# Performance work log

Measured on AMD Instinct MI355X. Metric: run time of the kernel, lower is better.

## Reference

```python
import jax, jax.numpy as jnp
import numpy as np

B, T, C = 8, 1024, 1024
EPS = 1e-5
NEG_INF = -1e38


def layernorm(x, w, b):
    mu = jnp.mean(x, axis=-1, keepdims=True)
    var = jnp.var(x, axis=-1, keepdims=True)
    return (x - mu) * jax.lax.rsqrt(var + EPS) * w + b


def wkv_scan(w, u, k, v):
    """Numerically-stable RWKV-4 WKV recurrence (forward direction).
    w: [C] (negative decay), u: [C] bonus, k, v: [B, T, C]. Returns [B, T, C]."""
    kt = jnp.swapaxes(k, 0, 1)  # [T, B, C]
    vt = jnp.swapaxes(v, 0, 1)
    bsz = k.shape[0]
    a0 = jnp.zeros((bsz, C), k.dtype)
    b0 = jnp.zeros((bsz, C), k.dtype)
    p0 = jnp.full((bsz, C), NEG_INF, k.dtype)

    def step(carry, inp):
        a, b, p = carry
        kk, vv = inp
        # output at current step (with bonus u on current token)
        q = jnp.maximum(p, u + kk)
        e1 = jnp.exp(p - q)
        e2 = jnp.exp(u + kk - q)
        out = (e1 * a + e2 * vv) / (e1 * b + e2)
        # decay state and absorb current token
        q2 = jnp.maximum(p + w, kk)
        f1 = jnp.exp(p + w - q2)
        f2 = jnp.exp(kk - q2)
        return (f1 * a + f2 * vv, f1 * b + f2, q2), out

    _, outs = jax.lax.scan(step, (a0, b0, p0), (kt, vt))
    return jnp.swapaxes(outs, 0, 1)  # [B, T, C]


def setup_inputs() -> dict:
    key = jax.random.key(0)
    ks = jax.random.split(key, 12)
    s = 0.02
    d = {}
    d["x"] = jax.random.normal(ks[0], (B, T, C), jnp.float32)
    d["ln1_w"] = jnp.ones((C,), jnp.float32)
    d["ln1_b"] = jnp.zeros((C,), jnp.float32)
    d["ln2_w"] = jnp.ones((C,), jnp.float32)
    d["ln2_b"] = jnp.zeros((C,), jnp.float32)
    d["Wr"] = jax.random.normal(ks[1], (C, C), jnp.float32) * s
    d["Wk"] = jax.random.normal(ks[2], (C, C), jnp.float32) * s
    d["Wv"] = jax.random.normal(ks[3], (C, C), jnp.float32) * s
    d["Wo"] = jax.random.normal(ks[4], (C, C), jnp.float32) * s
    d["decay"] = jax.random.normal(ks[5], (C,), jnp.float32) * 0.1
    d["u"] = jax.random.normal(ks[6], (C,), jnp.float32) * 0.1
    d["Wfk"] = jax.random.normal(ks[7], (4 * C, C), jnp.float32) * s
    d["Wfv"] = jax.random.normal(ks[8], (C, 4 * C), jnp.float32) * s
    d["Wfr"] = jax.random.normal(ks[9], (C, C), jnp.float32) * s
    return d


def reference(x, ln1_w, ln1_b, ln2_w, ln2_b, Wr, Wk, Wv, Wo, decay, u, Wfk, Wfv, Wfr):
    # --- bidirectional time-mix (WKV attention) ---
    xn = layernorm(x, ln1_w, ln1_b)
    r = jax.nn.sigmoid(xn @ Wr.T)
    k = xn @ Wk.T
    v = xn @ Wv.T
    w = -jnp.exp(decay)  # per-channel negative decay
    wkv_f = wkv_scan(w, u, k, v)
    wkv_b = jnp.flip(wkv_scan(w, u, jnp.flip(k, axis=1), jnp.flip(v, axis=1)), axis=1)
    wkv = 0.5 * (wkv_f + wkv_b)
    x = x + (r * wkv) @ Wo.T
    # --- channel-mix FFN ---
    xn2 = layernorm(x, ln2_w, ln2_b)
    kk = jnp.square(jax.nn.relu(xn2 @ Wfk.T))  # [B, T, 4C]
    x = x + jax.nn.sigmoid(xn2 @ Wfr.T) * (kk @ Wfv.T)
    return x
```

## Files before the change

### kernel.cpp

```cpp
#include <hip/hip_runtime.h>
#include <cstdint>
#include <cstddef>

typedef unsigned short u16;
typedef unsigned char u8;
typedef unsigned int u32;
typedef __bf16 bf16_t;
typedef bf16_t bf16x8 __attribute__((ext_vector_type(8)));
typedef float f32x4 __attribute__((ext_vector_type(4)));
typedef int i32x8 __attribute__((ext_vector_type(8)));

#define GCH 16
#define TCH 64

static __device__ __forceinline__ float bf2f(u16 v) {
    union { unsigned int u; float f; } cv;
    cv.u = ((unsigned int)v) << 16;
    return cv.f;
}
static __device__ __forceinline__ u16 f2bf(float f) {
    union { float f; unsigned int u; } cv;
    cv.f = f;
    unsigned int r = 0x7fffu + ((cv.u >> 16) & 1u);
    return (u16)((cv.u + r) >> 16);
}

#define SBAR() do { __builtin_amdgcn_sched_barrier(0); \
                    __builtin_amdgcn_s_barrier();      \
                    __builtin_amdgcn_sched_barrier(0); } while (0)

struct WSegs { const float* src[7]; void* dst[7]; int n4[7]; int mode[7]; };

__global__ __launch_bounds__(256)
void wconv_all(WSegs s)
{
    const int seg = blockIdx.y;
    const int i = blockIdx.x * 256 + threadIdx.x;
    if (i >= s.n4[seg]) return;
    float4 f = ((const float4*)s.src[seg])[i];
    if (s.mode[seg] == 0) {
        ushort4 o;
        o.x = f2bf(f.x); o.y = f2bf(f.y); o.z = f2bf(f.z); o.w = f2bf(f.w);
        ((ushort4*)s.dst[seg])[i] = o;
    } else {
        const int p0 = __builtin_amdgcn_cvt_pk_fp8_f32(f.x * 16.f, f.y * 16.f, 0, 0);
        const int p1 = __builtin_amdgcn_cvt_pk_fp8_f32(f.z * 16.f, f.w * 16.f, 0, 0);
        ((u32*)s.dst[seg])[i] = (u32)(p0 & 0xFFFF) | ((u32)p1 << 16);
    }
}

template<int BF16IN, int OUT8>
__global__ __launch_bounds__(256)
void ln_kernel(const void* __restrict__ xin, const float* __restrict__ w,
               const float* __restrict__ b, void* __restrict__ out)
{
    const int row = blockIdx.x;
    const int tid = threadIdx.x;
    float vals[4];
    if (BF16IN) {
        const ushort4 uv = ((const ushort4*)((const u16*)xin + (size_t)row * 1024))[tid];
        vals[0] = bf2f(uv.x); vals[1] = bf2f(uv.y);
        vals[2] = bf2f(uv.z); vals[3] = bf2f(uv.w);
    } else {
        const float4 f = ((const float4*)((const float*)xin + (size_t)row * 1024))[tid];
        vals[0] = f.x; vals[1] = f.y; vals[2] = f.z; vals[3] = f.w;
    }
    float s  = vals[0] + vals[1] + vals[2] + vals[3];
    float ss = vals[0]*vals[0] + vals[1]*vals[1] + vals[2]*vals[2] + vals[3]*vals[3];
    for (int off = 32; off; off >>= 1) {
        s  += __shfl_down(s, off, 64);
        ss += __shfl_down(ss, off, 64);
    }
    __shared__ float redS[4], redQ[4];
    if ((tid & 63) == 0) { redS[tid >> 6] = s; redQ[tid >> 6] = ss; }
    __syncthreads();
    s  = redS[0] + redS[1] + redS[2] + redS[3];
    ss = redQ[0] + redQ[1] + redQ[2] + redQ[3];
    const float mu  = s * (1.f / 1024.f);
    const float var = ss * (1.f / 1024.f) - mu * mu;
    const float rs  = rsqrtf(var + 1e-5f);
    const float4 wv = ((const float4*)w)[tid];
    const float4 bv = ((const float4*)b)[tid];
    const float o0 = (vals[0] - mu) * rs * wv.x + bv.x;
    const float o1 = (vals[1] - mu) * rs * wv.y + bv.y;
    const float o2 = (vals[2] - mu) * rs * wv.z + bv.z;
    const float o3 = (vals[3] - mu) * rs * wv.w + bv.w;
    if (OUT8) {
        const int p0 = __builtin_amdgcn_cvt_pk_fp8_f32(o0, o1, 0, 0);
        const int p1 = __builtin_amdgcn_cvt_pk_fp8_f32(o2, o3, 0, 0);
        ((u32*)out)[(size_t)row * 256 + tid] = (u32)(p0 & 0xFFFF) | ((u32)p1 << 16);
    } else {
        ushort4 o;
        o.x = f2bf(o0); o.y = f2bf(o1); o.z = f2bf(o2); o.w = f2bf(o3);
        ((ushort4*)out)[(size_t)row * 256 + tid] = o;
    }
}

template<int EPI, int DBUF>
__global__ __launch_bounds__(256)
void gemm_bt(const u16* __restrict__ A, const u16* __restrict__ B,
             int M, int N, int K,
             void* __restrict__ outp,
             const void* __restrict__ aux1, const void* __restrict__ aux2)
{
    __shared__ u16 lA[(1 + DBUF) * 128 * 64];
    __shared__ u16 lB[(1 + DBUF) * 128 * 64];
    const int tid  = threadIdx.x;
    const int wave = tid >> 6;
    const int lane = tid & 63;
    const int q    = lane >> 4;
    const int l16  = lane & 15;
    const long mBase = (long)blockIdx.x * 128;
    const long nBase = (long)blockIdx.y * 128;
    const int wm = (wave >> 1) * 64;
    const int wn = (wave & 1) * 64;

    f32x4 acc[4][4];
#pragma unroll
    for (int i = 0; i < 4; ++i)
#pragma unroll
        for (int j = 0; j < 4; ++j)
#pragma unroll
            for (int r = 0; r < 4; ++r) acc[i][j][r] = 0.f;

    const int srow = tid >> 3;
    const int scol = ((tid & 7) ^ (srow & 7)) * 8;
    const int ldsW = wave * 512;
    const int swz = l16 & 7;

    if (DBUF == 0) {
        for (int kb = 0; kb < K; kb += 64) {
            __syncthreads();
#pragma unroll
            for (int c = 0; c < 4; ++c) {
                const int row = c * 32 + srow;
                const u16* ga = A + (mBase + row) * (long)K + kb + scol;
                const u16* gb = B + (nBase + row) * (long)K + kb + scol;
                __builtin_amdgcn_global_load_lds(
                    (const __attribute__((address_space(1))) void*)ga,
                    (__attribute__((address_space(3))) void*)(lA + c * 2048 + ldsW),
                    16, 0, 0);
                __builtin_amdgcn_global_load_lds(
                    (const __attribute__((address_space(1))) void*)gb,
                    (__attribute__((address_space(3))) void*)(lB + c * 2048 + ldsW),
                    16, 0, 0);
            }
            __syncthreads();
#pragma unroll
            for (int ks = 0; ks < 2; ++ks) {
                const int grp = ((ks * 4 + q) ^ swz) * 8;
                bf16x8 af[4], bfm[4];
#pragma unroll
                for (int i = 0; i < 4; ++i) {
                    af[i]  = *(const bf16x8*)(lA + (wm + i * 16 + l16) * 64 + grp);
                    bfm[i] = *(const bf16x8*)(lB + (wn + i * 16 + l16) * 64 + grp);
                }
#pragma unroll
                for (int i = 0; i < 4; ++i)
#pragma unroll
                    for (int j = 0; j < 4; ++j)
                        acc[i][j] = __builtin_amdgcn_mfma_f32_16x16x32_bf16(
                            af[i], bfm[j], acc[i][j], 0, 0, 0);
            }
        }
    } else {
        auto stage = [&](int kb, int bufsel) {
#pragma unroll
            for (int c = 0; c < 4; ++c) {
                const int row = c * 32 + srow;
                const u16* ga = A + (mBase + row) * (long)K + kb + scol;
                const u16* gb = B + (nBase + row) * (long)K + kb + scol;
                __builtin_amdgcn_global_load_lds(
                    (const __attribute__((address_space(1))) void*)ga,
                    (__attribute__((address_space(3))) void*)(lA + bufsel * 8192 + c * 2048 + ldsW),
                    16, 0, 0);
                __builtin_amdgcn_global_load_lds(
                    (const __attribute__((address_space(1))) void*)gb,
                    (__attribute__((address_space(3))) void*)(lB + bufsel * 8192 + c * 2048 + ldsW),
                    16, 0, 0);
            }
        };
        auto compute = [&](int bufsel) {
            const u16* bA = lA + bufsel * 8192;
            const u16* bB = lB + bufsel * 8192;
#pragma unroll
            for (int ks = 0; ks < 2; ++ks) {
                const int grp = ((ks * 4 + q) ^ swz) * 8;
                bf16x8 af[4], bfm[4];
#pragma unroll
                for (int i = 0; i < 4; ++i) {
                    af[i]  = *(const bf16x8*)(bA + (wm + i * 16 + l16) * 64 + grp);
                    bfm[i] = *(const bf16x8*)(bB + (wn + i * 16 + l16) * 64 + grp);
                }
#pragma unroll
                for (int i = 0; i < 4; ++i)
#pragma unroll
                    for (int j = 0; j < 4; ++j)
                        acc[i][j] = __builtin_amdgcn_mfma_f32_16x16x32_bf16(
                            af[i], bfm[j], acc[i][j], 0, 0, 0);
            }
        };

        const int nt = K >> 6;
        stage(0, 0);
        stage(64, 1);
        asm volatile("s_waitcnt vmcnt(8)" ::: "memory");
        SBAR();
        for (int t = 0; t < nt - 2; ++t) {
            compute(t & 1);
            SBAR();
            stage((t + 2) << 6, t & 1);
            asm volatile("s_waitcnt vmcnt(8)" ::: "memory");
            SBAR();
        }
        compute(nt & 1);
        asm volatile("s_waitcnt vmcnt(0)" ::: "memory");
        SBAR();
        compute((nt - 1) & 1);
    }

    if (EPI == 5) {
        const long seg = nBase >> 10;
        u16* optr = (u16*)(seg == 0 ? outp : seg == 1 ? (void*)aux1 : (void*)aux2);
        const long cb = (nBase & 1023) + wn + l16;
#pragma unroll
        for (int i = 0; i < 4; ++i)
#pragma unroll
            for (int r = 0; r < 4; ++r) {
                const long rowOff = (mBase + wm + i * 16 + q * 4 + r) * 1024 + cb;
#pragma unroll
                for (int j = 0; j < 4; ++j)
                    optr[rowOff + j * 16] = f2bf(acc[i][j][r]);
            }
    } else {
        const long colBase = nBase + wn + l16;
#pragma unroll
        for (int i = 0; i < 4; ++i) {
#pragma unroll
            for (int r = 0; r < 4; ++r) {
                const long row = mBase + wm + i * 16 + q * 4 + r;
                const long rowOff = row * (long)N;
#pragma unroll
                for (int j = 0; j < 4; ++j) {
                    const long idx = rowOff + colBase + j * 16;
                    const float val = acc[i][j][r];
                    if (EPI == 1) {
                        ((u16*)outp)[idx] = f2bf(((const float*)aux1)[idx] + val);
                    } else {
                        const float t = bf2f(((const u16*)aux1)[idx])
                                      + bf2f(((const u16*)aux2)[idx]) * val;
                        ((float*)outp)[idx] = t;
                    }
                }
            }
        }
    }
}

__global__ __launch_bounds__(256)
void gemm_f8(const u8* __restrict__ A, const u8* __restrict__ B,
             int M, int N, int K,
             u16* __restrict__ kk, u16* __restrict__ rp)
{
    __shared__ __align__(16) u8 lA[128 * 128];
    __shared__ __align__(16) u8 lB[128 * 128];
    const int tid  = threadIdx.x;
    const int wave = tid >> 6;
    const int lane = tid & 63;
    const int q    = lane >> 4;
    const int l16  = lane & 15;
    const long mBase = (long)blockIdx.x * 128;
    const long nBase = (long)blockIdx.y * 128;
    const int wm = (wave >> 1) * 64;
    const int wn = (wave & 1) * 64;

    f32x4 acc[4][4];
#pragma unroll
    for (int i = 0; i < 4; ++i)
#pragma unroll
        for (int j = 0; j < 4; ++j)
#pragma unroll
            for (int r = 0; r < 4; ++r) acc[i][j][r] = 0.f;

    const int srow  = tid >> 3;
    const int scolB = ((tid & 7) ^ (srow & 7)) * 16;
    const int ldsW  = wave * 1024;
    const int swz   = l16 & 7;

    for (int kb = 0; kb < K; kb += 128) {
        __syncthreads();
#pragma unroll
        for (int c = 0; c < 4; ++c) {
            const int row = c * 32 + srow;
            const u8* ga = A + (mBase + row) * (long)K + kb + scolB;
            const u8* gb = B + (nBase + row) * (long)K + kb + scolB;
            __builtin_amdgcn_global_load_lds(
                (const __attribute__((address_space(1))) void*)ga,
                (__attribute__((address_space(3))) void*)(lA + c * 4096 + ldsW),
                16, 0, 0);
            __builtin_amdgcn_global_load_lds(
                (const __attribute__((address_space(1))) void*)gb,
                (__attribute__((address_space(3))) void*)(lB + c * 4096 + ldsW),
                16, 0, 0);
        }
        __syncthreads();
        const int u0 = ((2 * q) ^ swz) * 16;
        const int u1 = ((2 * q + 1) ^ swz) * 16;
        i32x8 af[4], bfm[4];
#pragma unroll
        for (int i = 0; i < 4; ++i) {
            {
                const u8* base = lA + (wm + i * 16 + l16) * 128;
                const uint4 lo = *(const uint4*)(base + u0);
                const uint4 hi = *(const uint4*)(base + u1);
                af[i][0] = lo.x; af[i][1] = lo.y; af[i][2] = lo.z; af[i][3] = lo.w;
                af[i][4] = hi.x; af[i][5] = hi.y; af[i][6] = hi.z; af[i][7] = hi.w;
            }
            {
                const u8* base = lB + (wn + i * 16 + l16) * 128;
                const uint4 lo = *(const uint4*)(base + u0);
                const uint4 hi = *(const uint4*)(base + u1);
                bfm[i][0] = lo.x; bfm[i][1] = lo.y; bfm[i][2] = lo.z; bfm[i][3] = lo.w;
                bfm[i][4] = hi.x; bfm[i][5] = hi.y; bfm[i][6] = hi.z; bfm[i][7] = hi.w;
            }
        }
#pragma unroll
        for (int i = 0; i < 4; ++i)
#pragma unroll
            for (int j = 0; j < 4; ++j)
                acc[i][j] = __builtin_amdgcn_mfma_scale_f32_16x16x128_f8f6f4(
                    af[i], bfm[j], acc[i][j], 0, 0, 0, 127, 0, 123);
    }

    u16* optr; long sN, cb;
    if (nBase < 4096) { optr = kk; sN = 4096; cb = nBase + wn + l16; }
    else              { optr = rp; sN = 1024; cb = (nBase - 4096) + wn + l16; }
#pragma unroll
    for (int i = 0; i < 4; ++i)
#pragma unroll
        for (int r = 0; r < 4; ++r) {
            const long rowOff = (mBase + wm + i * 16 + q * 4 + r) * sN + cb;
#pragma unroll
            for (int j = 0; j < 4; ++j) {
                const float val = acc[i][j][r];
                float t;
                if (nBase < 4096) t = val > 0.f ? val * val : 0.f;
                else t = __fdividef(1.f, 1.f + __expf(-val));
                optr[rowOff + j * 16] = f2bf(t);
            }
        }
}

__global__ __launch_bounds__(64)
void wkv_sum(const u16* __restrict__ kbuf, const u16* __restrict__ vbuf,
             const float* __restrict__ decay,
             float* __restrict__ sumA, float* __restrict__ sumB,
             float* __restrict__ sumP)
{
    const int c   = blockIdx.x * 64 + threadIdx.x;
    const int bt  = blockIdx.y;
    const int dir = blockIdx.z & 1;
    const int g   = blockIdx.z >> 1;
    const long base = (long)bt * (1024 * 1024) + c;
    const long stride = dir ? -1024 : 1024;
    long idx = dir ? base + (long)(1023 - g * TCH) * 1024
                   : base + (long)(g * TCH) * 1024;
    const float w = -__expf(decay[c]);
    float a = 0.f, b = 0.f, p = -1e38f;

    float kq[8], vq[8];
#pragma unroll
    for (int j = 0; j < 8; ++j) {
        kq[j] = bf2f(kbuf[idx + j * stride]);
        vq[j] = bf2f(vbuf[idx + j * stride]);
    }
    for (int tb = 0; tb < TCH / 8; ++tb) {
        float kn[8], vn[8];
        if (tb < TCH / 8 - 1) {
#pragma unroll
            for (int j = 0; j < 8; ++j) {
                kn[j] = bf2f(kbuf[idx + (j + 8) * stride]);
                vn[j] = bf2f(vbuf[idx + (j + 8) * stride]);
            }
        }
#pragma unroll
        for (int j = 0; j < 8; ++j) {
            const float kk = kq[j], vv = vq[j];
            const float pw = p + w;
            const float d  = pw - kk;
            const float e  = __expf(-fabsf(d));
            const float f1 = d >= 0.f ? 1.f : e;
            const float f2 = d >= 0.f ? e : 1.f;
            a = f1 * a + f2 * vv;
            b = f1 * b + f2;
            p = fmaxf(pw, kk);
        }
#pragma unroll
        for (int j = 0; j < 8; ++j) { kq[j] = kn[j]; vq[j] = vn[j]; }
        idx += 8 * stride;
    }
    const int sidx = (((dir * GCH + g) * 8 + bt) << 10) + c;
    sumA[sidx] = a; sumB[sidx] = b; sumP[sidx] = p;
}

__global__ __launch_bounds__(64)
void wkv_out2(const u16* __restrict__ kbuf, const u16* __restrict__ vbuf,
              const float* __restrict__ decay, const float* __restrict__ uarr,
              const float* __restrict__ sumA, const float* __restrict__ sumB,
              const float* __restrict__ sumP,
              const u16* __restrict__ rpre, u16* __restrict__ rwkv)
{
    __shared__ float fbuf[TCH * 64];
    const int lane = threadIdx.x;
    const int c   = blockIdx.x * 64 + lane;
    const int bt  = blockIdx.y;
    const int g   = blockIdx.z;
    const long base = (long)bt * (1024 * 1024) + c;
    const long rowBase = base + (long)(g * TCH) * 1024;
    const float w  = -__expf(decay[c]);
    const float uu = uarr[c];

    {
        float a = 0.f, b = 0.f, p = -1e38f;
        for (int gg = 0; gg < g; ++gg) {
            const int sidx = ((gg * 8 + bt) << 10) + c;
            const float a2 = sumA[sidx], b2 = sumB[sidx], p2 = sumP[sidx];
            const float pd = p + w * (float)TCH;
            const float d  = pd - p2;
            const float e  = __expf(-fabsf(d));
            const float x1 = d >= 0.f ? 1.f : e;
            const float x2 = d >= 0.f ? e : 1.f;
            a = x1 * a + x2 * a2;
            b = x1 * b + x2 * b2;
            p = fmaxf(pd, p2);
        }
        long idx = rowBase;
        float kq[8], vq[8];
#pragma unroll
        for (int j = 0; j < 8; ++j) {
            kq[j] = bf2f(kbuf[idx + j * 1024]);
            vq[j] = bf2f(vbuf[idx + j * 1024]);
        }
        for (int tb = 0; tb < TCH / 8; ++tb) {
            float kn[8], vn[8];
            if (tb < TCH / 8 - 1) {
#pragma unroll
                for (int j = 0; j < 8; ++j) {
                    kn[j] = bf2f(kbuf[idx + (j + 8) * 1024]);
                    vn[j] = bf2f(vbuf[idx + (j + 8) * 1024]);
                }
            }
#pragma unroll
            for (int j = 0; j < 8; ++j) {
                const float kk = kq[j], vv = vq[j];
                const float uk = uu + kk;
                const float d1 = p - uk;
                const float e  = __expf(-fabsf(d1));
                const float e1 = d1 >= 0.f ? 1.f : e;
                const float e2 = d1 >= 0.f ? e : 1.f;
                fbuf[(tb * 8 + j) * 64 + lane] =
                    __fdividef(e1 * a + e2 * vv, e1 * b + e2);
                const float pw = p + w;
                const float d2 = pw - kk;
                const float e_ = __expf(-fabsf(d2));
                const float f1 = d2 >= 0.f ? 1.f : e_;
                const float f2 = d2 >= 0.f ? e_ : 1.f;
                a = f1 * a + f2 * vv;
                b = f1 * b + f2;
                p = fmaxf(pw, kk);
            }
#pragma unroll
            for (int j = 0; j < 8; ++j) { kq[j] = kn[j]; vq[j] = vn[j]; }
            idx += 8 * 1024;
        }
    }
    __syncthreads();

    {
        float a = 0.f, b = 0.f, p = -1e38f;
        const int gb = GCH - 1 - g;
        for (int gg = 0; gg < gb; ++gg) {
            const int sidx = (((GCH + gg) * 8 + bt) << 10) + c;
            const float a2 = sumA[sidx], b2 = sumB[sidx], p2 = sumP[sidx];
            const float pd = p + w * (float)TCH;
            const float d  = pd - p2;
            const float e  = __expf(-fabsf(d));
            const float x1 = d >= 0.f ? 1.f : e;
            const float x2 = d >= 0.f ? e : 1.f;
            a = x1 * a + x2 * a2;
            b = x1 * b + x2 * b2;
            p = fmaxf(pd, p2);
        }
        long idx = rowBase + (long)(TCH - 1) * 1024;
        float kq[8], vq[8];
#pragma unroll
        for (int j = 0; j < 8; ++j) {
            kq[j] = bf2f(kbuf[idx - j * 1024]);
            vq[j] = bf2f(vbuf[idx - j * 1024]);
        }
        for (int tb = 0; tb < TCH / 8; ++tb) {
            float kn[8], vn[8];
            if (tb < TCH / 8 - 1) {
#pragma unroll
                for (int j = 0; j < 8; ++j) {
                    kn[j] = bf2f(kbuf[idx - (j + 8) * 1024]);
                    vn[j] = bf2f(vbuf[idx - (j + 8) * 1024]);
                }
            }
#pragma unroll
            for (int j = 0; j < 8; ++j) {
                const long ii = idx - (long)j * 1024;
                const int  tl = TCH - 1 - (tb * 8 + j);
                const float kk = kq[j], vv = vq[j];
                const float uk = uu + kk;
                const float d1 = p - uk;
                const float e  = __expf(-fabsf(d1));
                const float e1 = d1 >= 0.f ? 1.f : e;
                const float e2 = d1 >= 0.f ? e : 1.f;
                const float ob = __fdividef(e1 * a + e2 * vv, e1 * b + e2);
                const float of = fbuf[tl * 64 + lane];
                const float rr = __fdividef(1.f, 1.f + __expf(-bf2f(rpre[ii])));
                rwkv[ii] = f2bf(rr * 0.5f * (of + ob));
                const float pw = p + w;
                const float d2 = pw - kk;
                const float e_ = __expf(-fabsf(d2));
                const float f1 = d2 >= 0.f ? 1.f : e_;
                const float f2 = d2 >= 0.f ? e_ : 1.f;
                a = f1 * a + f2 * vv;
                b = f1 * b + f2;
                p = fmaxf(pw, kk);
            }
#pragma unroll
            for (int j = 0; j < 8; ++j) { kq[j] = kn[j]; vq[j] = vn[j]; }
            idx -= 8 * 1024;
        }
    }
}

extern "C" void kernel_launch(void* const* d_in, const int* in_sizes, int n_in,
                              void* d_out, int out_size, void* d_ws, size_t ws_size,
                              hipStream_t stream)
{
    (void)in_sizes; (void)n_in; (void)out_size; (void)ws_size;
    const float* x     = (const float*)d_in[0];
    const float* ln1w  = (const float*)d_in[1];
    const float* ln1b  = (const float*)d_in[2];
    const float* ln2w  = (const float*)d_in[3];
    const float* ln2b  = (const float*)d_in[4];
    const float* Wr    = (const float*)d_in[5];
    const float* Wk    = (const float*)d_in[6];
    const float* Wv    = (const float*)d_in[7];
    const float* Wo    = (const float*)d_in[8];
    const float* decay = (const float*)d_in[9];
    const float* uarr  = (const float*)d_in[10];
    const float* Wfk   = (const float*)d_in[11];
    const float* Wfv   = (const float*)d_in[12];
    const float* Wfr   = (const float*)d_in[13];

    const int M = 8192, C = 1024, C4 = 4096;
    const size_t MB = 1024u * 1024u;
    char* ws = (char*)d_ws;
    u16*  X2    = (u16*)(ws);
    u16*  XN    = (u16*)(ws + 16 * MB);
    u8*   XN8   = (u8*)(ws + 16 * MB);
    u16*  RP    = (u16*)(ws + 32 * MB);
    u16*  KB    = (u16*)(ws + 48 * MB);
    u16*  VB    = (u16*)(ws + 64 * MB);
    u16*  RWKV  = (u16*)(ws + 80 * MB);
    u16*  KK    = (u16*)(ws + 48 * MB);
    float* sumA = (float*)(ws + 112 * MB);
    float* sumB = (float*)(ws + 113 * MB);
    float* sumP = (float*)(ws + 114 * MB);
    u16*  WrB   = (u16*)(ws + 116 * MB);
    u16*  WkB   = (u16*)(ws + 118 * MB);
    u16*  WvB   = (u16*)(ws + 120 * MB);
    u16*  WoB   = (u16*)(ws + 122 * MB);
    u8*   Wf8   = (u8*)(ws + 124 * MB);
    u8*   Wfr8  = (u8*)(ws + 128 * MB);
    u16*  WfvB  = (u16*)(ws + 130 * MB);

    const dim3 blk(256);
    const int n4_1M = C * C / 4, n4_4M = C * C4 / 4;

    WSegs segs;
    segs.src[0] = Wr;  segs.dst[0] = WrB;  segs.n4[0] = n4_1M; segs.mode[0] = 0;
    segs.src[1] = Wk;  segs.dst[1] = WkB;  segs.n4[1] = n4_1M; segs.mode[1] = 0;
    segs.src[2] = Wv;  segs.dst[2] = WvB;  segs.n4[2] = n4_1M; segs.mode[2] = 0;
    segs.src[3] = Wo;  segs.dst[3] = WoB;  segs.n4[3] = n4_1M; segs.mode[3] = 0;
    segs.src[4] = Wfk; segs.dst[4] = Wf8;  segs.n4[4] = n4_4M; segs.mode[4] = 1;
    segs.src[5] = Wfr; segs.dst[5] = Wfr8; segs.n4[5] = n4_1M; segs.mode[5] = 1;
    segs.src[6] = Wfv; segs.dst[6] = WfvB; segs.n4[6] = n4_4M; segs.mode[6] = 0;
    wconv_all<<<dim3(n4_4M / 256, 7), blk, 0, stream>>>(segs);

    ln_kernel<0, 0><<<dim3(M), blk, 0, stream>>>(x, ln1w, ln1b, XN);
    gemm_bt<5, 1><<<dim3(M / 128, 3 * C / 128), blk, 0, stream>>>(
        XN, WrB, M, 3 * C, C, RP, KB, VB);
    wkv_sum<<<dim3(16, 8, 2 * GCH), dim3(64), 0, stream>>>(KB, VB, decay,
                                                           sumA, sumB, sumP);
    wkv_out2<<<dim3(16, 8, GCH), dim3(64), 0, stream>>>(KB, VB, decay, uarr,
                                                        sumA, sumB, sumP,
                                                        RP, RWKV);
    gemm_bt<1, 1><<<dim3(M / 128, C / 128), blk, 0, stream>>>(
        RWKV, WoB, M, C, C, X2, x, nullptr);
    ln_kernel<1, 1><<<dim3(M), blk, 0, stream>>>(X2, ln2w, ln2b, XN8);
    gemm_f8<<<dim3(M / 128, 5 * C / 128), blk, 0, stream>>>(
        XN8, Wf8, M, 5 * C, C, KK, RP);
    gemm_bt<4, 1><<<dim3(M / 128, C / 128), blk, 0, stream>>>(
        KK, WfvB, M, C, C4, d_out, X2, RP);
}
```

Baseline: 418.5 us.

## Select per-GEMM K-loop pipelining variants and drop sched barriers

Splits the bf16 GEMM main loop into template-selected variants. DBUF=1 becomes a simple two-buffer loop that stages the next tile before computing the current one, with __syncthreads between steps. Other DBUF values keep the vmcnt-gated prefetch-two pipeline, now using plain s_barrier without sched_barrier fences. The QKV GEMM switches to DBUF=0, which presumably means a smaller shared-memory footprint and higher occupancy. The FFN down-projection switches to the explicit vmcnt pipeline. The trade-off is less load/compute overlap and freer compiler scheduling, which may reorder memory operations in ways that hurt latency hiding.

```diff
diff --git a/kernel.cpp b/kernel.cpp
--- a/kernel.cpp
+++ b/kernel.cpp
@@ -24,10 +24,6 @@
     unsigned int r = 0x7fffu + ((cv.u >> 16) & 1u);
     return (u16)((cv.u + r) >> 16);
 }
-
-#define SBAR() do { __builtin_amdgcn_sched_barrier(0); \
-                    __builtin_amdgcn_s_barrier();      \
-                    __builtin_amdgcn_sched_barrier(0); } while (0)
 
 struct WSegs { const float* src[7]; void* dst[7]; int n4[7]; int mode[7]; };
 
@@ -103,8 +99,8 @@
              void* __restrict__ outp,
              const void* __restrict__ aux1, const void* __restrict__ aux2)
 {
-    __shared__ u16 lA[(1 + DBUF) * 128 * 64];
-    __shared__ u16 lB[(1 + DBUF) * 128 * 64];
+    __shared__ u16 lA[(DBUF ? 2 : 1) * 128 * 64];
+    __shared__ u16 lB[(DBUF ? 2 : 1) * 128 * 64];
     const int tid  = threadIdx.x;
     const int wave = tid >> 6;
     const int lane = tid & 63;
@@ -201,22 +197,40 @@
             }
         };
 
-        const int nt = K >> 6;
-        stage(0, 0);
-        stage(64, 1);
-        asm volatile("s_waitcnt vmcnt(8)" ::: "memory");
-        SBAR();
-        for (int t = 0; t < nt - 2; ++t) {
-            compute(t & 1);
-            SBAR();
-            stage((t + 2) << 6, t & 1);
+        if (DBUF == 1) {
+            stage(0, 0);
+            __syncthreads();
+            int cur = 0;
+            for (int kb = 0; kb < K; kb += 64) {
+                if (kb + 64 < K) stage(kb + 64, cur ^ 1);
+                compute(cur);
+                __syncthreads();
+                cur ^= 1;
+            }
+        } else {
+            const int nt = K >> 6;
+            stage(0, 0);
+            stage(64, 1);
             asm volatile("s_waitcnt vmcnt(8)" ::: "memory");
-            SBAR();
-        }
-        compute(nt & 1);
-        asm volatile("s_waitcnt vmcnt(0)" ::: "memory");
-        SBAR();
-        compute((nt - 1) & 1);
+            __builtin_amdgcn_s_barrier();
+            asm volatile("" ::: "memory");
+            int cur = 0;
+            for (int t = 0; t < nt - 2; ++t) {
+                compute(cur);
+                __builtin_amdgcn_s_barrier();
+                asm volatile("" ::: "memory");
+                stage((t + 2) << 6, cur);
+                asm volatile("s_waitcnt vmcnt(8)" ::: "memory");
+                __builtin_amdgcn_s_barrier();
+                asm volatile("" ::: "memory");
+                cur ^= 1;
+            }
+            compute(cur);
+            asm volatile("s_waitcnt vmcnt(0)" ::: "memory");
+            __builtin_amdgcn_s_barrier();
+            asm volatile("" ::: "memory");
+            compute(cur ^ 1);
+        }
     }
 
     if (EPI == 5) {
@@ -593,7 +607,7 @@
     wconv_all<<<dim3(n4_4M / 256, 7), blk, 0, stream>>>(segs);
 
     ln_kernel<0, 0><<<dim3(M), blk, 0, stream>>>(x, ln1w, ln1b, XN);
-    gemm_bt<5, 1><<<dim3(M / 128, 3 * C / 128), blk, 0, stream>>>(
+    gemm_bt<5, 0><<<dim3(M / 128, 3 * C / 128), blk, 0, stream>>>(
         XN, WrB, M, 3 * C, C, RP, KB, VB);
     wkv_sum<<<dim3(16, 8, 2 * GCH), dim3(64), 0, stream>>>(KB, VB, decay,
                                                            sumA, sumB, sumP);
@@ -605,6 +619,6 @@
     ln_kernel<1, 1><<<dim3(M), blk, 0, stream>>>(X2, ln2w, ln2b, XN8);
     gemm_f8<<<dim3(M / 128, 5 * C / 128), blk, 0, stream>>>(
         XN8, Wf8, M, 5 * C, C, KK, RP);
-    gemm_bt<4, 1><<<dim3(M / 128, C / 128), blk, 0, stream>>>(
+    gemm_bt<4, 2><<<dim3(M / 128, C / 128), blk, 0, stream>>>(
         KK, WfvB, M, C, C4, d_out, X2, RP);
 }
```

After: 411.0 us. About the same (-1.8%).
